# Kernel optimization log

Hardware: AMD Instinct MI355X
Metric: run time of the kernel (lower is better)

## Reference

```python
import jax, jax.numpy as jnp
import numpy as np

WS, STRIDE, GRID, HW = 3, 2, 4, 9          # window, stride, 4x4 windows, 9x9 grid
HEADS, HEAD_DIM, DIM = 4, 16, 64
INNER = HEADS * HEAD_DIM                    # 64
BATCH = 8192

_RI = (np.arange(GRID) * STRIDE)[:, None] + np.arange(WS)[None, :]   # [4,3] row/col starts+offsets
_coords = np.array([[x, y] for x in range(WS) for y in range(WS)])   # [9,2]
_REL = (_coords[None, :, :] - _coords[:, None, :]) + (WS - 1)        # [9,9,2] in [0,4]


def setup_inputs() -> dict:
    key = jax.random.key(0)
    ks = jax.random.split(key, 6)
    return {
        "x": jax.random.normal(ks[0], (BATCH, HW, HW, DIM), jnp.float32),
        "w_qkv": jax.random.normal(ks[1], (3 * INNER, DIM), jnp.float32) * 0.05,
        "pos_embedding": jax.random.normal(ks[2], (2 * WS - 1, 2 * WS - 1), jnp.float32),
        "w1": jax.random.normal(ks[3], (DIM // 2, INNER), jnp.float32) * 0.05,
        "b1": jnp.zeros((DIM // 2,), jnp.float32),
        "ln_g": jnp.ones((DIM // 2,), jnp.float32),
        "ln_b": jnp.zeros((DIM // 2,), jnp.float32),
        "w2": jax.random.normal(ks[4], (DIM, DIM // 2), jnp.float32) * 0.05,
        "b2": jnp.zeros((DIM,), jnp.float32),
    }


def reference(x, w_qkv, pos_embedding, w1, b1, ln_g, ln_b, w2, b2):
    b = x.shape[0]
    ri = jnp.asarray(_RI)                                  # [4,3]
    rel0 = jnp.asarray(_REL[..., 0]); rel1 = jnp.asarray(_REL[..., 1])

    qkv = jnp.einsum('bhwc,oc->bhwo', x, w_qkv)            # [b,9,9,3*INNER]
    # nn.Unfold(k=3, s=2): overlapping 3x3 windows -> [b,4,4,3,3,3I] -> [b,16,9,3I]
    win = qkv[:, ri[:, None, :, None], ri[None, :, None, :], :]
    win = win.reshape(b, GRID * GRID, WS * WS, 3 * INNER)
    q, k, v = jnp.split(win, 3, axis=-1)

    def to_heads(t):  # [b,n,wh,(h d)] -> [b,h,n,wh,d]
        return t.reshape(b, GRID * GRID, WS * WS, HEADS, HEAD_DIM).transpose(0, 3, 1, 2, 4)
    q, k, v = to_heads(q), to_heads(k), to_heads(v)

    bias = pos_embedding[rel0, rel1]                       # [9,9] relative-position bias
    attn = jnp.einsum('bhwid,bhwjd->bhwij', q, k) * (HEAD_DIM ** -0.5) + bias
    attn = jax.nn.softmax(attn, axis=-1)
    out = jnp.einsum('bhwij,bhwjd->bhwid', attn, v)        # [b,H,16,9,D]

    # rearrange 'b h n wh d -> b (wh h d) n'
    outf = out.transpose(0, 3, 1, 4, 2).reshape(b, WS * WS * INNER, GRID * GRID)
    # nn.Fold interprets channels as (c, kernel_pos) with c = idx // 9; overlaps are summed
    tmp = outf.reshape(b, INNER, WS, WS, GRID, GRID).transpose(0, 4, 5, 2, 3, 1)  # [b,wi,wj,ki,kj,C]
    canvas = jnp.zeros((b, HW, HW, INNER), out.dtype)
    canvas = canvas.at[:, ri[:, None, :, None], ri[None, :, None, :], :].add(tmp)

    h1 = jnp.einsum('bhwc,oc->bhwo', canvas, w1) + b1      # Linear(inner, dim/2)
    mu = jnp.mean(h1, -1, keepdims=True)
    var = jnp.var(h1, -1, keepdims=True)
    h1 = (h1 - mu) * jax.lax.rsqrt(var + 1e-5) * ln_g + ln_b
    h1 = jax.nn.gelu(h1, approximate=False)                # torch nn.GELU default = exact erf
    return jnp.einsum('bhwc,oc->bhwo', h1, w2) + b2        # [b,9,9,DIM]
```

## Files before the change

### kernel.cpp

```cpp
#include <hip/hip_runtime.h>
#include <math.h>

#define BLOCK_ 512
#define BPB_   8
#define NBLK_  (8192/BPB_)

typedef __bf16 bf16x8 __attribute__((ext_vector_type(8)));
typedef float  f32x4  __attribute__((ext_vector_type(4)));
typedef unsigned short us8 __attribute__((ext_vector_type(8)));

#define XS_  72
#define QKS_ 136
#define VS_  72
#define CS_  68
#define W1S_ 72
#define W2S_ 40
#define HGS_ 40

struct alignas(16) Smem {
    unsigned short Xb[81*XS_];
    unsigned short QK[81*QKS_];
    unsigned short Vf[81*VS_];
    float          Cv[81*CS_];
    unsigned short W1[32*W1S_];
    unsigned short W2[64*W2S_];
    float Bias[81];
    float B1v[32], LnG[32], LnB[32], B2v[64];
};

__device__ __forceinline__ unsigned short f2bf(float f) {
    union { float f; unsigned u; } v; v.f = f;
    unsigned r = v.u + 0x7FFFu + ((v.u >> 16) & 1u);
    return (unsigned short)(r >> 16);
}
__device__ __forceinline__ float bf2f(unsigned short b) {
    union { float f; unsigned u; } v; v.u = ((unsigned)b) << 16;
    return v.f;
}
__device__ __forceinline__ us8 pack8(float4 a, float4 b) {
    us8 r;
    r[0]=f2bf(a.x); r[1]=f2bf(a.y); r[2]=f2bf(a.z); r[3]=f2bf(a.w);
    r[4]=f2bf(b.x); r[5]=f2bf(b.y); r[6]=f2bf(b.z); r[7]=f2bf(b.w);
    return r;
}
__device__ __forceinline__ f32x4 mfma16(us8 a, us8 b, f32x4 c) {
    return __builtin_amdgcn_mfma_f32_16x16x32_bf16(
        __builtin_bit_cast(bf16x8, a), __builtin_bit_cast(bf16x8, b), c, 0, 0, 0);
}

__global__ __launch_bounds__(BLOCK_, 2)
void wattn_mfma(const float* __restrict__ x, const float* __restrict__ w_qkv,
                const float* __restrict__ pe, const float* __restrict__ w1,
                const float* __restrict__ b1, const float* __restrict__ lng,
                const float* __restrict__ lnb, const float* __restrict__ w2,
                const float* __restrict__ b2, float* __restrict__ out)
{
    __shared__ Smem sm;
    const int t = threadIdx.x;
    const int wv = t >> 6, lane = t & 63;
    const int lrow = lane & 15;
    const int lk   = (lane >> 4) * 8;
    const int g4   = (lane >> 4) * 4;
    const int ng = wv & 3, mg = wv >> 2;

    for (int task = t; task < 32*8; task += BLOCK_) {
        int p = task >> 3, c8 = task & 7;
        const float4* src = (const float4*)(w1 + p*64 + c8*8);
        *(us8*)&sm.W1[p*W1S_ + c8*8] = pack8(src[0], src[1]);
    }
    for (int task = t; task < 64*4; task += BLOCK_) {
        int p = task >> 2, c8 = task & 3;
        const float4* src = (const float4*)(w2 + p*32 + c8*8);
        *(us8*)&sm.W2[p*W2S_ + c8*8] = pack8(src[0], src[1]);
    }
    if (t < 32) { sm.B1v[t]=b1[t]; sm.LnG[t]=lng[t]; sm.LnB[t]=lnb[t]; }
    if (t >= 64 && t < 128) sm.B2v[t-64] = b2[t-64];
    if (t >= 128 && t < 209) {
        int ij = t-128; int i = ij/9, j = ij%9;
        sm.Bias[ij] = pe[((j/3)-(i/3)+2)*5 + ((j%3)-(i%3)+2)];
    }
    for (int idx = t; idx < 81*CS_; idx += BLOCK_) sm.Cv[idx] = 0.f;
    {
        const float* xb = x + (size_t)blockIdx.x * BPB_ * (81*64);
        for (int task = t; task < 648; task += BLOCK_) {
            int p = task >> 3, c8 = task & 7;
            const float4* src = (const float4*)(xb + p*64 + c8*8);
            *(us8*)&sm.Xb[p*XS_ + c8*8] = pack8(src[0], src[1]);
        }
    }
    __syncthreads();

    for (int bi = 0; bi < BPB_; ++bi) {
        const size_t b = (size_t)blockIdx.x * BPB_ + bi;
        const bool hasPF = (bi + 1 < BPB_);
        const bool hasPF2 = hasPF && (t < 136);

        {
            us8 bq[3][2];
            #pragma unroll
            for (int ni = 0; ni < 3; ++ni)
                #pragma unroll
                for (int k = 0; k < 2; ++k) {
                    const float4* src = (const float4*)(w_qkv + ((ng*3+ni)*16 + lrow)*64 + k*32 + lk);
                    bq[ni][k] = pack8(src[0], src[1]);
                }
            us8 af[3][2];
            #pragma unroll
            for (int mi = 0; mi < 3; ++mi) {
                const int arow = min(mg*48 + mi*16 + lrow, 80);
                #pragma unroll
                for (int k = 0; k < 2; ++k)
                    af[mi][k] = *(const us8*)&sm.Xb[arow*XS_ + k*32 + lk];
            }
            #pragma unroll
            for (int ni = 0; ni < 3; ++ni) {
                const int n = ng*3 + ni;
                f32x4 acc[3];
                #pragma unroll
                for (int mi = 0; mi < 3; ++mi) {
                    acc[mi][0]=0.f; acc[mi][1]=0.f; acc[mi][2]=0.f; acc[mi][3]=0.f;
                }
                #pragma unroll
                for (int k = 0; k < 2; ++k)
                    #pragma unroll
                    for (int mi = 0; mi < 3; ++mi)
                        acc[mi] = mfma16(af[mi][k], bq[ni][k], acc[mi]);
                #pragma unroll
                for (int mi = 0; mi < 3; ++mi) {
                    const int row0 = mg*48 + mi*16 + g4;
                    if (n < 8) {
                        #pragma unroll
                        for (int r = 0; r < 4; ++r) {
                            int row = row0 + r;
                            if (row < 81) sm.QK[row*QKS_ + n*16 + lrow] = f2bf(acc[mi][r]);
                        }
                    } else {
                        #pragma unroll
                        for (int r = 0; r < 4; ++r) {
                            int row = row0 + r;
                            if (row < 81) sm.Vf[row*VS_ + (n-8)*16 + lrow] = f2bf(acc[mi][r]);
                        }
                    }
                }
            }
        }
        __syncthreads();

        for (int task = t; task < 576; task += BLOCK_) {
            int w = task/36, rem = task%36, h = rem/9, i = rem%9;
            int r0 = (w>>2)*2, c0 = (w&3)*2;
            int posq = (r0 + i/3)*9 + (c0 + i%3);
            float q[16];
            {
                us8 u0 = *(const us8*)&sm.QK[posq*QKS_ + h*16];
                us8 u1 = *(const us8*)&sm.QK[posq*QKS_ + h*16 + 8];
                #pragma unroll
                for (int jj=0;jj<8;++jj){ q[jj]=bf2f(u0[jj]); q[8+jj]=bf2f(u1[jj]); }
            }
            float l[9]; float mx = -1e30f;
            #pragma unroll
            for (int j = 0; j < 9; ++j) {
                int posk = (r0 + j/3)*9 + (c0 + j%3);
                us8 u0 = *(const us8*)&sm.QK[posk*QKS_ + 64 + h*16];
                us8 u1 = *(const us8*)&sm.QK[posk*QKS_ + 64 + h*16 + 8];
                float s = 0.f;
                #pragma unroll
                for (int jj=0;jj<8;++jj) s += q[jj]*bf2f(u0[jj]) + q[8+jj]*bf2f(u1[jj]);
                l[j] = s*0.25f + sm.Bias[i*9+j];
                mx = fmaxf(mx, l[j]);
            }
            float ssum = 0.f;
            #pragma unroll
            for (int j=0;j<9;++j){ l[j]=__expf(l[j]-mx); ssum+=l[j]; }
            float inv = 1.f/ssum;
            float o[16];
            #pragma unroll
            for (int d=0; d<16; ++d) o[d]=0.f;
            #pragma unroll
            for (int j = 0; j < 9; ++j) {
                float a = l[j]*inv;
                int posv = (r0 + j/3)*9 + (c0 + j%3);
                us8 v0 = *(const us8*)&sm.Vf[posv*VS_ + h*16];
                us8 v1 = *(const us8*)&sm.Vf[posv*VS_ + h*16 + 8];
                #pragma unroll
                for (int jj=0;jj<8;++jj) {
                    o[jj]   += a * bf2f(v0[jj]);
                    o[8+jj] += a * bf2f(v1[jj]);
                }
            }
            int base576 = i*64 + h*16;
            #pragma unroll
            for (int d=0; d<16; ++d) {
                int idx = base576 + d;
                int c = idx/9, r = idx - 9*c;
                int row = (r0 + r/3)*9 + (c0 + r%3);
                atomicAdd(&sm.Cv[row*CS_ + c], o[d]);
            }
        }
        __syncthreads();

        float4 pA0, pA1, pB0, pB1;
        if (hasPF) {
            const float4* xn = (const float4*)(x + (b+1)*(81*64));
            pA0 = xn[t*2]; pA1 = xn[t*2+1];
            if (hasPF2) { pB0 = xn[(512+t)*2]; pB1 = xn[(512+t)*2+1]; }
        }

        if (wv < 6) {
            const int m = wv;
            const int arow = m*16 + lrow;
            us8 aF[2];
            #pragma unroll
            for (int k = 0; k < 2; ++k) {
                #pragma unroll
                for (int e=0;e<8;++e) aF[k][e] = 0;
                if (arow < 81) {
                    const float* cp = &sm.Cv[arow*CS_ + k*32 + lk];
                    aF[k] = pack8(*(const float4*)cp, *(const float4*)(cp+4));
                }
            }
            f32x4 a0, a1;
            a0[0]=0.f; a0[1]=0.f; a0[2]=0.f; a0[3]=0.f;
            a1[0]=0.f; a1[1]=0.f; a1[2]=0.f; a1[3]=0.f;
            #pragma unroll
            for (int k = 0; k < 2; ++k) {
                us8 b0  = *(const us8*)&sm.W1[lrow*W1S_ + k*32 + lk];
                us8 b1f = *(const us8*)&sm.W1[(16+lrow)*W1S_ + k*32 + lk];
                a0 = mfma16(aF[k], b0, a0);
                a1 = mfma16(aF[k], b1f, a1);
            }
            float bb0 = sm.B1v[lrow], bb1 = sm.B1v[16+lrow];
            float gg0 = sm.LnG[lrow], gg1 = sm.LnG[16+lrow];
            float ee0 = sm.LnB[lrow], ee1 = sm.LnB[16+lrow];
            float v0[4], v1[4], srow[4], qrow[4];
            #pragma unroll
            for (int r=0;r<4;++r) {
                v0[r] = a0[r] + bb0; v1[r] = a1[r] + bb1;
                srow[r] = v0[r] + v1[r];
                qrow[r] = v0[r]*v0[r] + v1[r]*v1[r];
            }
            #pragma unroll
            for (int mask = 1; mask <= 8; mask <<= 1)
                #pragma unroll
                for (int r=0;r<4;++r) {
                    srow[r] += __shfl_xor(srow[r], mask);
                    qrow[r] += __shfl_xor(qrow[r], mask);
                }
            unsigned short* H1g = sm.QK;
            #pragma unroll
            for (int r=0;r<4;++r) {
                int row = m*16 + g4 + r;
                if (row < 81) {
                    float mean = srow[r]*(1.f/32.f);
                    float var  = qrow[r]*(1.f/32.f) - mean*mean;
                    float rs   = rsqrtf(var + 1e-5f);
                    float xn0 = (v0[r]-mean)*rs*gg0 + ee0;
                    float xn1 = (v1[r]-mean)*rs*gg1 + ee1;
                    float ge0 = 0.5f*xn0*(1.f + erff(xn0*0.70710678118654752f));
                    float ge1 = 0.5f*xn1*(1.f + erff(xn1*0.70710678118654752f));
                    H1g[row*HGS_ + lrow]      = f2bf(ge0);
                    H1g[row*HGS_ + 16 + lrow] = f2bf(ge1);
                }
            }
        }
        __syncthreads();

        {
            const unsigned short* H1g = sm.QK;
            #pragma unroll
            for (int ti = 0; ti < 3; ++ti) {
                int ft = wv*3 + ti;
                int m = ft >> 2, n = ft & 3;
                int arow = m*16 + lrow;
                us8 aH;
                #pragma unroll
                for (int e=0;e<8;++e) aH[e] = 0;
                if (arow < 81) aH = *(const us8*)&H1g[arow*HGS_ + lk];
                us8 bW = *(const us8*)&sm.W2[(n*16+lrow)*W2S_ + lk];
                f32x4 zz;
                zz[0]=0.f; zz[1]=0.f; zz[2]=0.f; zz[3]=0.f;
                f32x4 acc = mfma16(aH, bW, zz);
                float bb = sm.B2v[n*16+lrow];
                int row0 = m*16 + g4;
                #pragma unroll
                for (int r=0;r<4;++r) {
                    int row = row0 + r;
                    if (row < 81)
                        out[(b*81 + (size_t)row)*64 + n*16 + lrow] = acc[r] + bb;
                }
            }
        }
        if (hasPF) {
            int p = t >> 3, c8 = t & 7;
            *(us8*)&sm.Xb[p*XS_ + c8*8] = pack8(pA0, pA1);
            if (hasPF2) {
                int task = 512 + t; p = task >> 3; c8 = task & 7;
                *(us8*)&sm.Xb[p*XS_ + c8*8] = pack8(pB0, pB1);
            }
        }
        for (int idx = t; idx < 81*CS_; idx += BLOCK_) sm.Cv[idx] = 0.f;
        __syncthreads();
    }
}

extern "C" void kernel_launch(void* const* d_in, const int* in_sizes, int n_in,
                              void* d_out, int out_size, void* d_ws, size_t ws_size,
                              hipStream_t stream) {
    const float* x     = (const float*)d_in[0];
    const float* w_qkv = (const float*)d_in[1];
    const float* pe    = (const float*)d_in[2];
    const float* w1    = (const float*)d_in[3];
    const float* b1    = (const float*)d_in[4];
    const float* lng   = (const float*)d_in[5];
    const float* lnb   = (const float*)d_in[6];
    const float* w2    = (const float*)d_in[7];
    const float* b2    = (const float*)d_in[8];
    float* outp = (float*)d_out;

    wattn_mfma<<<dim3(NBLK_), dim3(BLOCK_), 0, stream>>>(
        x, w_qkv, pe, w1, b1, lng, lnb, w2, b2, outp);
}
```

Measured before the change: 679.3 us.

## Compute window attention with MFMA per window-head and wave-shuffle softmax

Replaces the per-thread scalar attention loop (one query row per thread, 576 tasks over 512 threads) with an MFMA-based scheme. Each wave handles 8 window-head pairs: one MFMA computes the 9x9 scores, a cross-lane shuffle softmax normalises them, and a second MFMA multiplies P by V. The weight fragments for the QKV projection are also loaded per column tile instead of all at once, to cut register pressure. Most of each 16x16 MFMA is padding for 9x9 tiles, and rounding P to bf16 adds some error.

```diff
diff --git a/kernel.cpp b/kernel.cpp
--- a/kernel.cpp
+++ b/kernel.cpp
@@ -42,6 +42,14 @@
     r[0]=f2bf(a.x); r[1]=f2bf(a.y); r[2]=f2bf(a.z); r[3]=f2bf(a.w);
     r[4]=f2bf(b.x); r[5]=f2bf(b.y); r[6]=f2bf(b.z); r[7]=f2bf(b.w);
     return r;
+}
+__device__ __forceinline__ us8 zero8() {
+    us8 z;
+    for (int e = 0; e < 8; ++e) z[e] = 0;
+    return z;
+}
+__device__ __forceinline__ f32x4 zero4() {
+    f32x4 z; z[0]=0.f; z[1]=0.f; z[2]=0.f; z[3]=0.f; return z;
 }
 __device__ __forceinline__ f32x4 mfma16(us8 a, us8 b, f32x4 c) {
     return __builtin_amdgcn_mfma_f32_16x16x32_bf16(
@@ -59,8 +67,9 @@
     const int t = threadIdx.x;
     const int wv = t >> 6, lane = t & 63;
     const int lrow = lane & 15;
-    const int lk   = (lane >> 4) * 8;
-    const int g4   = (lane >> 4) * 4;
+    const int g    = lane >> 4;
+    const int lk   = g * 8;
+    const int g4   = g * 4;
     const int ng = wv & 3, mg = wv >> 2;
 
     for (int task = t; task < 32*8; task += BLOCK_) {
@@ -96,14 +105,6 @@
         const bool hasPF2 = hasPF && (t < 136);
 
         {
-            us8 bq[3][2];
-            #pragma unroll
-            for (int ni = 0; ni < 3; ++ni)
-                #pragma unroll
-                for (int k = 0; k < 2; ++k) {
-                    const float4* src = (const float4*)(w_qkv + ((ng*3+ni)*16 + lrow)*64 + k*32 + lk);
-                    bq[ni][k] = pack8(src[0], src[1]);
-                }
             us8 af[3][2];
             #pragma unroll
             for (int mi = 0; mi < 3; ++mi) {
@@ -115,16 +116,20 @@
             #pragma unroll
             for (int ni = 0; ni < 3; ++ni) {
                 const int n = ng*3 + ni;
+                us8 bq[2];
+                #pragma unroll
+                for (int k = 0; k < 2; ++k) {
+                    const float4* src = (const float4*)(w_qkv + (n*16 + lrow)*64 + k*32 + lk);
+                    bq[k] = pack8(src[0], src[1]);
+                }
                 f32x4 acc[3];
                 #pragma unroll
-                for (int mi = 0; mi < 3; ++mi) {
-                    acc[mi][0]=0.f; acc[mi][1]=0.f; acc[mi][2]=0.f; acc[mi][3]=0.f;
-                }
+                for (int mi = 0; mi < 3; ++mi) acc[mi] = zero4();
                 #pragma unroll
                 for (int k = 0; k < 2; ++k)
                     #pragma unroll
                     for (int mi = 0; mi < 3; ++mi)
-                        acc[mi] = mfma16(af[mi][k], bq[ni][k], acc[mi]);
+                        acc[mi] = mfma16(af[mi][k], bq[k], acc[mi]);
                 #pragma unroll
                 for (int mi = 0; mi < 3; ++mi) {
                     const int row0 = mg*48 + mi*16 + g4;
@@ -146,55 +151,63 @@
         }
         __syncthreads();
 
-        for (int task = t; task < 576; task += BLOCK_) {
-            int w = task/36, rem = task%36, h = rem/9, i = rem%9;
-            int r0 = (w>>2)*2, c0 = (w&3)*2;
-            int posq = (r0 + i/3)*9 + (c0 + i%3);
-            float q[16];
-            {
-                us8 u0 = *(const us8*)&sm.QK[posq*QKS_ + h*16];
-                us8 u1 = *(const us8*)&sm.QK[posq*QKS_ + h*16 + 8];
-                #pragma unroll
-                for (int jj=0;jj<8;++jj){ q[jj]=bf2f(u0[jj]); q[8+jj]=bf2f(u1[jj]); }
-            }
-            float l[9]; float mx = -1e30f;
-            #pragma unroll
-            for (int j = 0; j < 9; ++j) {
-                int posk = (r0 + j/3)*9 + (c0 + j%3);
-                us8 u0 = *(const us8*)&sm.QK[posk*QKS_ + 64 + h*16];
-                us8 u1 = *(const us8*)&sm.QK[posk*QKS_ + 64 + h*16 + 8];
-                float s = 0.f;
-                #pragma unroll
-                for (int jj=0;jj<8;++jj) s += q[jj]*bf2f(u0[jj]) + q[8+jj]*bf2f(u1[jj]);
-                l[j] = s*0.25f + sm.Bias[i*9+j];
-                mx = fmaxf(mx, l[j]);
-            }
-            float ssum = 0.f;
-            #pragma unroll
-            for (int j=0;j<9;++j){ l[j]=__expf(l[j]-mx); ssum+=l[j]; }
-            float inv = 1.f/ssum;
-            float o[16];
-            #pragma unroll
-            for (int d=0; d<16; ++d) o[d]=0.f;
-            #pragma unroll
-            for (int j = 0; j < 9; ++j) {
-                float a = l[j]*inv;
-                int posv = (r0 + j/3)*9 + (c0 + j%3);
-                us8 v0 = *(const us8*)&sm.Vf[posv*VS_ + h*16];
-                us8 v1 = *(const us8*)&sm.Vf[posv*VS_ + h*16 + 8];
-                #pragma unroll
-                for (int jj=0;jj<8;++jj) {
-                    o[jj]   += a * bf2f(v0[jj]);
-                    o[8+jj] += a * bf2f(v1[jj]);
-                }
-            }
-            int base576 = i*64 + h*16;
-            #pragma unroll
-            for (int d=0; d<16; ++d) {
-                int idx = base576 + d;
-                int c = idx/9, r = idx - 9*c;
-                int row = (r0 + r/3)*9 + (c0 + r%3);
-                atomicAdd(&sm.Cv[row*CS_ + c], o[d]);
+        #pragma unroll
+        for (int u = 0; u < 8; ++u) {
+            const int pp = (wv << 3) | u;
+            const int w = pp >> 2, h = pp & 3;
+            const int base = (w >> 2) * 18 + (w & 3) * 2;
+            const int cc  = min(lrow, 8);
+            const int pos = base + (cc/3)*9 + (cc - (cc/3)*3);
+            us8 aK = zero8(), bQ = zero8();
+            if (g < 2) {
+                aK = *(const us8*)&sm.QK[pos*QKS_ + 64 + h*16 + lk];
+                bQ = *(const us8*)&sm.QK[pos*QKS_ + h*16 + lk];
+            }
+            f32x4 s4 = mfma16(aK, bQ, zero4());
+            const int ib = cc * 9;
+            float raw[4];
+            #pragma unroll
+            for (int r = 0; r < 4; ++r) {
+                int j = g4 + r;
+                raw[r] = (j < 9) ? s4[r]*0.25f + sm.Bias[ib + j] : -1e30f;
+            }
+            float mx = fmaxf(fmaxf(raw[0], raw[1]), fmaxf(raw[2], raw[3]));
+            mx = fmaxf(mx, __shfl_xor(mx, 16));
+            mx = fmaxf(mx, __shfl_xor(mx, 32));
+            float ex[4]; float sum = 0.f;
+            #pragma unroll
+            for (int r = 0; r < 4; ++r) { ex[r] = __expf(raw[r] - mx); sum += ex[r]; }
+            sum += __shfl_xor(sum, 16);
+            sum += __shfl_xor(sum, 32);
+            const float inv = 1.f / sum;
+            float pf[4];
+            #pragma unroll
+            for (int r = 0; r < 4; ++r) pf[r] = ex[r] * inv;
+            float pg0 = __shfl_xor(pf[0], 16), pg1 = __shfl_xor(pf[1], 16);
+            float pg2 = __shfl_xor(pf[2], 16), pg3 = __shfl_xor(pf[3], 16);
+            float p8  = __shfl_xor(pf[0], 48);
+            us8 a2 = zero8(), b2 = zero8();
+            if (g == 0) {
+                a2[0]=f2bf(pf[0]); a2[1]=f2bf(pf[1]); a2[2]=f2bf(pf[2]); a2[3]=f2bf(pf[3]);
+                a2[4]=f2bf(pg0);  a2[5]=f2bf(pg1);  a2[6]=f2bf(pg2);  a2[7]=f2bf(pg3);
+                const unsigned short* vb = &sm.Vf[base*VS_ + h*16 + lrow];
+                b2[0]=vb[0];       b2[1]=vb[VS_];     b2[2]=vb[2*VS_];
+                b2[3]=vb[9*VS_];   b2[4]=vb[10*VS_];  b2[5]=vb[11*VS_];
+                b2[6]=vb[18*VS_];  b2[7]=vb[19*VS_];
+            } else if (g == 1) {
+                a2[0] = f2bf(p8);
+                b2[0] = sm.Vf[(base+20)*VS_ + h*16 + lrow];
+            }
+            f32x4 o4 = mfma16(a2, b2, zero4());
+            #pragma unroll
+            for (int r = 0; r < 4; ++r) {
+                int i = g4 + r;
+                if (i < 9) {
+                    int idx = i*64 + h*16 + lrow;
+                    int c = idx/9, rr = idx - 9*c;
+                    int row = base + (rr/3)*9 + (rr - (rr/3)*3);
+                    atomicAdd(&sm.Cv[row*CS_ + c], o4[r]);
+                }
             }
         }
         __syncthreads();
@@ -212,16 +225,13 @@
             us8 aF[2];
             #pragma unroll
             for (int k = 0; k < 2; ++k) {
-                #pragma unroll
-                for (int e=0;e<8;++e) aF[k][e] = 0;
+                aF[k] = zero8();
                 if (arow < 81) {
                     const float* cp = &sm.Cv[arow*CS_ + k*32 + lk];
                     aF[k] = pack8(*(const float4*)cp, *(const float4*)(cp+4));
                 }
             }
-            f32x4 a0, a1;
-            a0[0]=0.f; a0[1]=0.f; a0[2]=0.f; a0[3]=0.f;
-            a1[0]=0.f; a1[1]=0.f; a1[2]=0.f; a1[3]=0.f;
+            f32x4 a0 = zero4(), a1 = zero4();
             #pragma unroll
             for (int k = 0; k < 2; ++k) {
                 us8 b0  = *(const us8*)&sm.W1[lrow*W1S_ + k*32 + lk];
@@ -272,14 +282,10 @@
                 int ft = wv*3 + ti;
                 int m = ft >> 2, n = ft & 3;
                 int arow = m*16 + lrow;
-                us8 aH;
-                #pragma unroll
-                for (int e=0;e<8;++e) aH[e] = 0;
+                us8 aH = zero8();
                 if (arow < 81) aH = *(const us8*)&H1g[arow*HGS_ + lk];
                 us8 bW = *(const us8*)&sm.W2[(n*16+lrow)*W2S_ + lk];
-                f32x4 zz;
-                zz[0]=0.f; zz[1]=0.f; zz[2]=0.f; zz[3]=0.f;
-                f32x4 acc = mfma16(aH, bW, zz);
+                f32x4 acc = mfma16(aH, bW, zero4());
                 float bb = sm.B2v[n*16+lrow];
                 int row0 = m*16 + g4;
                 #pragma unroll
```

Result: slower. 719.6 us (+5.9%).
